# Kernel tuning notes

Measured on AMD Instinct MI355X. Metric: run time of the kernel, lower is better.

Reference implementation:

```python
import jax, jax.numpy as jnp
import numpy as np

N = 50000
E = 400000
D = 128            # embedding_dim
NUM_RBF = 20
CUT_OFF = 5.0
SILU_SCALE = 1.0 / 0.6


def scaled_silu(x):
    return jax.nn.silu(x) * SILU_SCALE


def cosine_cutoff(x):
    return 0.5 * (1.0 + jnp.cos(x * jnp.pi / CUT_OFF)) * (x < CUT_OFF).astype(x.dtype)


def setup_inputs() -> dict:
    key = jax.random.key(0)
    ks = jax.random.split(key, 10)
    vectorial_feat = jax.random.normal(ks[0], (N, D, 3), dtype=jnp.float32)
    scalar_feat = jax.random.normal(ks[1], (N, D), dtype=jnp.float32)
    node_pos = jax.random.uniform(ks[2], (N, 3), dtype=jnp.float32) * 10.0
    source = jax.random.randint(ks[3], (E,), 0, N)
    offset = jax.random.randint(ks[4], (E,), 1, N)  # avoid self-loops -> no zero distance
    target = (source + offset) % N
    edge_index = jnp.stack([source, target], axis=0).astype(jnp.int64)
    # scalar_feat_proj: Linear(D,D) -> ScaledSiLU -> Linear(D, 3D)
    W1 = jax.random.normal(ks[5], (D, D), dtype=jnp.float32) * (1.0 / np.sqrt(D))
    b1 = jnp.zeros((D,), dtype=jnp.float32)
    W2 = jax.random.normal(ks[6], (D, 3 * D), dtype=jnp.float32) * (1.0 / np.sqrt(D))
    b2 = jnp.zeros((3 * D,), dtype=jnp.float32)
    # rbf_proj: Linear(NUM_RBF, 3D)
    Wr = jax.random.normal(ks[7], (NUM_RBF, 3 * D), dtype=jnp.float32) * (1.0 / np.sqrt(NUM_RBF))
    br = jnp.zeros((3 * D,), dtype=jnp.float32)
    return {"vectorial_feat": vectorial_feat, "scalar_feat": scalar_feat,
            "node_pos": node_pos, "edge_index": edge_index,
            "W1": W1, "b1": b1, "W2": W2, "b2": b2, "Wr": Wr, "br": br}


def reference(vectorial_feat, scalar_feat, node_pos, edge_index, W1, b1, W2, b2, Wr, br):
    freqs = jnp.arange(1, NUM_RBF + 1, dtype=jnp.float32) * jnp.pi  # [NUM_RBF]
    source, target = edge_index[0], edge_index[1]

    # node-level scalar projection: [N, 3D]
    s = scaled_silu(scalar_feat @ W1 + b1) @ W2 + b2

    # per-edge geometry
    rel = node_pos[target] - node_pos[source]                 # [E, 3]
    dist = jnp.sqrt(jnp.sum(rel * rel, axis=-1))              # [E]
    dist_scaled = dist / CUT_OFF
    rbf = jnp.sin(freqs[None, :] * dist_scaled[:, None]) / dist[:, None]  # [E, NUM_RBF]

    filt = cosine_cutoff(rbf @ Wr + br)                       # [E, 3D]

    message = (s[source] * filt).reshape(E, D, 3)             # [E, D, 3]
    scalar_msg = message[..., 0]                              # [E, D]
    equiv_msg = message[..., 1]                               # [E, D]
    invar_msg = message[..., 2]                               # [E, D]

    scalar_message = jax.ops.segment_sum(scalar_msg, target, num_segments=N)  # [N, D]

    direction = rel / dist[:, None]                           # [E, 3]
    vec_msg = (invar_msg[:, :, None] * direction[:, None, :]
               + equiv_msg[:, :, None] * vectorial_feat[source])  # [E, D, 3]
    vectorial_message = jax.ops.segment_sum(vec_msg, target, num_segments=N)  # [N, D, 3]

    return vectorial_message, scalar_message
```

## Files before the change

### kernel.cpp

```cpp
#include <hip/hip_runtime.h>
#include <hip/hip_fp16.h>
#include <math.h>
#include <stddef.h>

#define D_DIM 128
#define NUM_RBF 20
typedef unsigned short ushort_t;
typedef unsigned int uint_t;
typedef _Float16 h2v __attribute__((ext_vector_type(2)));
typedef _Float16 half8_t __attribute__((ext_vector_type(8)));
typedef float float4_t __attribute__((ext_vector_type(4)));
constexpr float PI_F = 3.14159265358979323846f;
constexpr float CUT_OFF_F = 5.0f;
constexpr float SILU_SCALE_F = 1.0f / 0.6f;

__device__ __forceinline__ uint_t pack2h(float a, float b) {
  __half2 h2 = __floats2half2_rn(a, b);
  return *reinterpret_cast<uint_t*>(&h2);
}
__device__ __forceinline__ float h2f(ushort_t u) {
  __half h = __ushort_as_half(u);
  return __half2float(h);
}
__device__ __forceinline__ float h2f_lo(uint_t u) { return h2f((ushort_t)(u & 0xffffu)); }
__device__ __forceinline__ float h2f_hi(uint_t u) { return h2f((ushort_t)(u >> 16)); }
__device__ __forceinline__ h2v u2h2(uint_t u) {
  h2v r;
  __builtin_memcpy(&r, &u, 4);
  return r;
}

#if defined(__has_builtin)
#if __has_builtin(__builtin_amdgcn_fdot2)
#define HAVE_FDOT2 1
#endif
#endif

__device__ __forceinline__ float fdot2f(h2v a, h2v b, float c) {
#ifdef HAVE_FDOT2
  return __builtin_amdgcn_fdot2(a, b, c, false);
#else
  return c + (float)a.x * (float)b.x + (float)a.y * (float)b.y;
#endif
}

struct __align__(16) EdgeRec {
  uint_t rb[10];
  uint_t src;
  float dx, dy, dz;
  uint_t pad[2];
};

__device__ __forceinline__ void stage_wt(const float* __restrict__ W,
                                         _Float16* __restrict__ Wt, int t,
                                         int f4stride, int f4base) {
  const float4* Wv = reinterpret_cast<const float4*>(W);
#pragma unroll
  for (int i = 0; i < 8; ++i) {
    int pid = t + i * 256;
    int k = (pid >> 5) * 2;
    int nf = pid & 31;
    float4 a = Wv[(size_t)k * f4stride + f4base + nf];
    float4 b = Wv[(size_t)(k + 1) * f4stride + f4base + nf];
    const float av[4] = {a.x, a.y, a.z, a.w};
    const float bv[4] = {b.x, b.y, b.z, b.w};
    const int n0 = nf * 4;
#pragma unroll
    for (int j = 0; j < 4; ++j)
      *reinterpret_cast<uint_t*>(&Wt[(n0 + j) * 136 + k]) =
          pack2h(av[j], bv[j]);
  }
}

__global__ __launch_bounds__(256) void proj_kernel(
    const float* __restrict__ X, const float* __restrict__ W1,
    const float* __restrict__ b1, const float* __restrict__ W2,
    const float* __restrict__ b2, const float* __restrict__ vf,
    uint_t* __restrict__ merged, int* __restrict__ counts, int N) {
  __shared__ alignas(16) _Float16 smem[26112];
  _Float16* Xs = smem;
  _Float16* Wt = smem + 8704;

  const int t = threadIdx.x;
  const int w = t >> 6;
  const int l = t & 63;
  const int nb = blockIdx.x * 64;

  {
    int z = blockIdx.x * 256 + t;
    if (z < N) counts[z] = 0;
  }

  {
    const float4* Xv = reinterpret_cast<const float4*>(X);
#pragma unroll
    for (int i = 0; i < 8; ++i) {
      int g = t + i * 256;
      int row = g >> 5, k0 = (g & 31) * 4;
      int node = nb + row;
      float4 v = (node < N) ? Xv[(size_t)nb * 32 + g]
                            : make_float4(0.f, 0.f, 0.f, 0.f);
      uint_t* dst = reinterpret_cast<uint_t*>(&Xs[row * 136 + k0]);
      dst[0] = pack2h(v.x, v.y);
      dst[1] = pack2h(v.z, v.w);
    }
  }
  stage_wt(W1, Wt, t, 32, 0);
  __syncthreads();

  const int arow = w * 16 + (l & 15);
  const int koff = (l >> 4) * 8;
  const int bcol = l & 15;

  half8_t af[4];
#pragma unroll
  for (int s = 0; s < 4; ++s)
    af[s] = *reinterpret_cast<const half8_t*>(&Xs[arow * 136 + s * 32 + koff]);

  float4_t acc[8];
#pragma unroll
  for (int c = 0; c < 8; ++c) {
    float4_t a = {0.f, 0.f, 0.f, 0.f};
#pragma unroll
    for (int s = 0; s < 4; ++s) {
      half8_t bf = *reinterpret_cast<const half8_t*>(
          &Wt[(c * 16 + bcol) * 136 + s * 32 + koff]);
      a = __builtin_amdgcn_mfma_f32_16x16x32_f16(af[s], bf, a, 0, 0, 0);
    }
    acc[c] = a;
  }

  __syncthreads();

#pragma unroll
  for (int c = 0; c < 8; ++c) {
    const int col = c * 16 + bcol;
    const float bv = b1[col];
#pragma unroll
    for (int r = 0; r < 4; ++r) {
      const int row = w * 16 + (l >> 4) * 4 + r;
      float hv = acc[c][r] + bv;
      hv = hv * SILU_SCALE_F / (1.0f + expf(-hv));
      Xs[row * 136 + col] = (_Float16)hv;
    }
  }
  stage_wt(W2, Wt, t, 96, 0);
  __syncthreads();

  half8_t ha[4];
#pragma unroll
  for (int s = 0; s < 4; ++s)
    ha[s] = *reinterpret_cast<const half8_t*>(&Xs[arow * 136 + s * 32 + koff]);

  uint_t pk[3][8][2];
#pragma unroll
  for (int cn = 0; cn < 3; ++cn) {
    if (cn > 0) {
      __syncthreads();
      stage_wt(W2, Wt, t, 96, cn * 32);
      __syncthreads();
    }
#pragma unroll
    for (int c = 0; c < 8; ++c) {
      float4_t a = {0.f, 0.f, 0.f, 0.f};
#pragma unroll
      for (int s = 0; s < 4; ++s) {
        half8_t bf = *reinterpret_cast<const half8_t*>(
            &Wt[(c * 16 + bcol) * 136 + s * 32 + koff]);
        a = __builtin_amdgcn_mfma_f32_16x16x32_f16(ha[s], bf, a, 0, 0, 0);
      }
      const float bv = b2[cn * 128 + c * 16 + bcol];
      pk[cn][c][0] = pack2h(a[0] + bv, a[1] + bv);
      pk[cn][c][1] = pack2h(a[2] + bv, a[3] + bv);
    }
  }

  __syncthreads();
  ushort_t* sh = reinterpret_cast<ushort_t*>(smem);
  {
    const int rbase = w * 16 + (l >> 4) * 4;
#pragma unroll
    for (int cn = 0; cn < 3; ++cn)
#pragma unroll
      for (int c = 0; c < 8; ++c) {
        const int gcol = cn * 128 + c * 16 + bcol;
        sh[(rbase + 0) * 392 + gcol] = (ushort_t)(pk[cn][c][0] & 0xffffu);
        sh[(rbase + 1) * 392 + gcol] = (ushort_t)(pk[cn][c][0] >> 16);
        sh[(rbase + 2) * 392 + gcol] = (ushort_t)(pk[cn][c][1] & 0xffffu);
        sh[(rbase + 3) * 392 + gcol] = (ushort_t)(pk[cn][c][1] >> 16);
      }
  }
  __syncthreads();

#pragma unroll
  for (int k = 0; k < 8; ++k) {
    const int P = k * 256 + t;
    const int ln = P >> 5;
    const int cg = (P & 31) * 4;
    const int node = nb + ln;
    if (node < N) {
      const ushort_t* sp = &sh[ln * 392 + 3 * cg];
      uint2 sa = *reinterpret_cast<const uint2*>(sp);
      uint2 sb = *reinterpret_cast<const uint2*>(sp + 4);
      uint2 sc = *reinterpret_cast<const uint2*>(sp + 8);
      ushort_t s12[12];
      s12[0] = (ushort_t)(sa.x & 0xffffu);  s12[1] = (ushort_t)(sa.x >> 16);
      s12[2] = (ushort_t)(sa.y & 0xffffu);  s12[3] = (ushort_t)(sa.y >> 16);
      s12[4] = (ushort_t)(sb.x & 0xffffu);  s12[5] = (ushort_t)(sb.x >> 16);
      s12[6] = (ushort_t)(sb.y & 0xffffu);  s12[7] = (ushort_t)(sb.y >> 16);
      s12[8] = (ushort_t)(sc.x & 0xffffu);  s12[9] = (ushort_t)(sc.x >> 16);
      s12[10] = (ushort_t)(sc.y & 0xffffu); s12[11] = (ushort_t)(sc.y >> 16);

      const float4* vp =
          reinterpret_cast<const float4*>(vf + ((size_t)node * 128 + cg) * 3);
      float4 v0 = vp[0], v1 = vp[1], v2 = vp[2];
      float vv[12] = {v0.x, v0.y, v0.z, v0.w, v1.x, v1.y,
                      v1.z, v1.w, v2.x, v2.y, v2.z, v2.w};

      uint_t o[12];
#pragma unroll
      for (int j = 0; j < 4; ++j) {
        o[3 * j + 0] = (uint_t)s12[3 * j] | ((uint_t)s12[3 * j + 1] << 16);
        o[3 * j + 1] =
            (uint_t)s12[3 * j + 2] |
            ((uint_t)__half_as_ushort(__float2half_rn(vv[3 * j])) << 16);
        o[3 * j + 2] = pack2h(vv[3 * j + 1], vv[3 * j + 2]);
      }
      uint_t* mp = merged + ((size_t)node * 128 + cg) * 3;
      *reinterpret_cast<uint4*>(mp) = make_uint4(o[0], o[1], o[2], o[3]);
      *reinterpret_cast<uint4*>(mp + 4) = make_uint4(o[4], o[5], o[6], o[7]);
      *reinterpret_cast<uint4*>(mp + 8) = make_uint4(o[8], o[9], o[10], o[11]);
    }
  }
}

__global__ void hist_kernel(const int* __restrict__ tgt, int* __restrict__ counts,
                            int E) {
  int e = blockIdx.x * 256 + threadIdx.x;
  if (e < E) atomicAdd(&counts[tgt[e]], 1);
}

__global__ void chunk_sum_kernel(const int* __restrict__ counts,
                                 int* __restrict__ chunk_sums, int N) {
  __shared__ int red[256];
  int b = blockIdx.x, t = threadIdx.x;
  int base = b * 1024 + t * 4;
  int s = 0;
#pragma unroll
  for (int j = 0; j < 4; ++j) s += (base + j < N) ? counts[base + j] : 0;
  red[t] = s;
  __syncthreads();
  for (int off = 128; off > 0; off >>= 1) {
    if (t < off) red[t] += red[t + off];
    __syncthreads();
  }
  if (t == 0) chunk_sums[b] = red[0];
}

__global__ void scan_block_kernel(const int* __restrict__ counts,
                                  const int* __restrict__ chunk_sums,
                                  int* __restrict__ offsets,
                                  int* __restrict__ cursor, int N, int E) {
  __shared__ int part[256];
  __shared__ int chunk_base_sh;
  int b = blockIdx.x, t = threadIdx.x;
  if (t < 64) {
    int v = (t < b) ? chunk_sums[t] : 0;
#pragma unroll
    for (int off = 32; off > 0; off >>= 1) v += __shfl_down(v, off);
    if (t == 0) chunk_base_sh = v;
  }
  int base = b * 1024 + t * 4;
  int v[4];
#pragma unroll
  for (int j = 0; j < 4; ++j) v[j] = (base + j < N) ? counts[base + j] : 0;
  int local = v[0] + v[1] + v[2] + v[3];
  part[t] = local;
  __syncthreads();
  for (int off = 1; off < 256; off <<= 1) {
    int x = 0;
    if (t >= off) x = part[t - off];
    __syncthreads();
    if (t >= off) part[t] += x;
    __syncthreads();
  }
  int run = chunk_base_sh + (part[t] - local);
#pragma unroll
  for (int j = 0; j < 4; ++j) {
    if (base + j < N) {
      offsets[base + j] = run;
      cursor[base + j] = run;
      run += v[j];
    }
  }
  if (b == 0 && t == 0) offsets[N] = E;
}

__global__ void edge_geom_kernel(const float* __restrict__ pos,
                                 const int* __restrict__ src,
                                 const int* __restrict__ tgt,
                                 int* __restrict__ cursor,
                                 EdgeRec* __restrict__ recs, int E) {
  int e = blockIdx.x * 256 + threadIdx.x;
  if (e >= E) return;
  const int sn = src[e];
  const int tn = tgt[e];
  const float rx = pos[tn * 3 + 0] - pos[sn * 3 + 0];
  const float ry = pos[tn * 3 + 1] - pos[sn * 3 + 1];
  const float rz = pos[tn * 3 + 2] - pos[sn * 3 + 2];
  const float dist = sqrtf(rx * rx + ry * ry + rz * rz);
  const float inv = 1.0f / dist;

  const float ang = dist * (PI_F / CUT_OFF_F);
  float s1, c1;
  sincosf(ang, &s1, &c1);
  float sk = s1, ck = c1;
  float rb[NUM_RBF];
  rb[0] = s1 * inv;
#pragma unroll
  for (int r = 1; r < NUM_RBF; ++r) {
    float sn2 = sk * c1 + ck * s1;
    ck = ck * c1 - sk * s1;
    sk = sn2;
    rb[r] = sk * inv;
  }

  const int p = atomicAdd(&cursor[tn], 1);
  uint_t us[10];
#pragma unroll
  for (int q = 0; q < 10; ++q) us[q] = pack2h(rb[2 * q], rb[2 * q + 1]);
  uint_t* o = reinterpret_cast<uint_t*>(&recs[p]);
  *reinterpret_cast<uint4*>(o) = make_uint4(us[0], us[1], us[2], us[3]);
  *reinterpret_cast<uint4*>(o + 4) = make_uint4(us[4], us[5], us[6], us[7]);
  *reinterpret_cast<uint4*>(o + 8) =
      make_uint4(us[8], us[9], (uint_t)sn, __float_as_uint(rx * inv));
  *reinterpret_cast<uint4*>(o + 12) =
      make_uint4(__float_as_uint(ry * inv), __float_as_uint(rz * inv), 0u, 0u);
}

#define NODES_PER_BLOCK 8

__device__ __forceinline__ float cutoff_f(float x) {
#if defined(__has_builtin)
#if __has_builtin(__builtin_amdgcn_cosf)
  float c = __builtin_amdgcn_cosf(x * 0.1f);
#else
  float c = __cosf(x * (PI_F / CUT_OFF_F));
#endif
#else
  float c = __cosf(x * (PI_F / CUT_OFF_F));
#endif
  return (x < CUT_OFF_F) ? 0.5f + 0.5f * c : 0.f;
}

__device__ __forceinline__ void edge_body(const EdgeRec& e, uint_t su0,
                                          uint_t su1, uint_t su2,
                                          const h2v* wr0h, const h2v* wr1h,
                                          const h2v* wr2h, float br0, float br1,
                                          float br2, float& accs, float& av0,
                                          float& av1, float& av2) {
  float f0 = br0, f1 = br1, f2 = br2;
#pragma unroll
  for (int q = 0; q < 10; ++q) {
    h2v r = u2h2(e.rb[q]);
    f0 = fdot2f(r, wr0h[q], f0);
    f1 = fdot2f(r, wr1h[q], f1);
    f2 = fdot2f(r, wr2h[q], f2);
  }
  f0 = cutoff_f(f0);
  f1 = cutoff_f(f1);
  f2 = cutoff_f(f2);
  const float m0 = h2f_lo(su0) * f0;
  const float m1 = h2f_hi(su0) * f1;
  const float m2 = h2f_lo(su1) * f2;
  accs += m0;
  av0 += m2 * e.dx + m1 * h2f_hi(su1);
  av1 += m2 * e.dy + m1 * h2f_lo(su2);
  av2 += m2 * e.dz + m1 * h2f_hi(su2);
}

__global__ __launch_bounds__(128) void node_kernel(
    const uint_t* __restrict__ merged, const EdgeRec* __restrict__ recs,
    const int* __restrict__ offsets, const float* __restrict__ Wr,
    const float* __restrict__ br, float* __restrict__ out, int N) {
  const int d = threadIdx.x;
  const int d3 = 3 * d;

  h2v wr0h[10], wr1h[10], wr2h[10];
#pragma unroll
  for (int q = 0; q < 10; ++q) {
    h2v w;
    w.x = (_Float16)Wr[(2 * q) * 384 + d3 + 0];
    w.y = (_Float16)Wr[(2 * q + 1) * 384 + d3 + 0];
    wr0h[q] = w;
    w.x = (_Float16)Wr[(2 * q) * 384 + d3 + 1];
    w.y = (_Float16)Wr[(2 * q + 1) * 384 + d3 + 1];
    wr1h[q] = w;
    w.x = (_Float16)Wr[(2 * q) * 384 + d3 + 2];
    w.y = (_Float16)Wr[(2 * q + 1) * 384 + d3 + 2];
    wr2h[q] = w;
  }
  const float br0 = br[d3 + 0];
  const float br1 = br[d3 + 1];
  const float br2 = br[d3 + 2];

  for (int nn = 0; nn < NODES_PER_BLOCK; ++nn) {
    const int n = blockIdx.x * NODES_PER_BLOCK + nn;
    if (n >= N) break;

    const int start = offsets[n];
    const int end = offsets[n + 1];

    float accs = 0.f, av0 = 0.f, av1 = 0.f, av2 = 0.f;

    int i = start;
    for (; i + 4 <= end; i += 4) {
      const int i0 = __builtin_amdgcn_readfirstlane(i);
      const EdgeRec& eA = recs[i0];
      const EdgeRec& eB = recs[i0 + 1];
      const EdgeRec& eC = recs[i0 + 2];
      const EdgeRec& eD = recs[i0 + 3];
      const uint_t* mpA = merged + (size_t)eA.src * 384 + d3;
      const uint_t* mpB = merged + (size_t)eB.src * 384 + d3;
      const uint_t* mpC = merged + (size_t)eC.src * 384 + d3;
      const uint_t* mpD = merged + (size_t)eD.src * 384 + d3;
      const uint_t suA0 = mpA[0], suA1 = mpA[1], suA2 = mpA[2];
      const uint_t suB0 = mpB[0], suB1 = mpB[1], suB2 = mpB[2];
      const uint_t suC0 = mpC[0], suC1 = mpC[1], suC2 = mpC[2];
      const uint_t suD0 = mpD[0], suD1 = mpD[1], suD2 = mpD[2];

      edge_body(eA, suA0, suA1, suA2, wr0h, wr1h, wr2h, br0, br1, br2, accs,
                av0, av1, av2);
      edge_body(eB, suB0, suB1, suB2, wr0h, wr1h, wr2h, br0, br1, br2, accs,
                av0, av1, av2);
      edge_body(eC, suC0, suC1, suC2, wr0h, wr1h, wr2h, br0, br1, br2, accs,
                av0, av1, av2);
      edge_body(eD, suD0, suD1, suD2, wr0h, wr1h, wr2h, br0, br1, br2, accs,
                av0, av1, av2);
    }
    for (; i < end; ++i) {
      const int i0 = __builtin_amdgcn_readfirstlane(i);
      const EdgeRec& eA = recs[i0];
      const uint_t* mpA = merged + (size_t)eA.src * 384 + d3;
      const uint_t suA0 = mpA[0], suA1 = mpA[1], suA2 = mpA[2];
      edge_body(eA, suA0, suA1, suA2, wr0h, wr1h, wr2h, br0, br1, br2, accs,
                av0, av1, av2);
    }

    out[(size_t)n * 384 + d3 + 0] = av0;
    out[(size_t)n * 384 + d3 + 1] = av1;
    out[(size_t)n * 384 + d3 + 2] = av2;
    out[(size_t)N * 384 + (size_t)n * 128 + d] = accs;
  }
}

extern "C" void kernel_launch(void* const* d_in, const int* in_sizes, int n_in,
                              void* d_out, int out_size, void* d_ws,
                              size_t ws_size, hipStream_t stream) {
  const float* vf  = (const float*)d_in[0];
  const float* X   = (const float*)d_in[1];
  const float* pos = (const float*)d_in[2];
  const int* ei    = (const int*)d_in[3];
  const float* W1  = (const float*)d_in[4];
  const float* b1  = (const float*)d_in[5];
  const float* W2  = (const float*)d_in[6];
  const float* b2  = (const float*)d_in[7];
  const float* Wr  = (const float*)d_in[8];
  const float* br  = (const float*)d_in[9];

  const int N = in_sizes[1] / D_DIM;
  const int E = in_sizes[3] / 2;
  const int* srcI = ei;
  const int* tgtI = ei + E;
  float* out = (float*)d_out;

  char* w = (char*)d_ws;
  EdgeRec* recs  = (EdgeRec*)w; w += (size_t)E * sizeof(EdgeRec);
  uint_t* merged = (uint_t*)w;  w += (size_t)N * 128 * 3 * sizeof(uint_t);
  int* counts    = (int*)w;     w += (size_t)N * sizeof(int);
  int* offsets   = (int*)w;     w += (size_t)(N + 1) * sizeof(int);
  int* cursor    = (int*)w;     w += (size_t)N * sizeof(int);
  int* chunks    = (int*)w;     w += 64 * sizeof(int);

  const int nch = (N + 1023) / 1024;

  proj_kernel<<<(N + 63) / 64, 256, 0, stream>>>(X, W1, b1, W2, b2, vf, merged,
                                                 counts, N);
  hist_kernel<<<(E + 255) / 256, 256, 0, stream>>>(tgtI, counts, E);
  chunk_sum_kernel<<<nch, 256, 0, stream>>>(counts, chunks, N);
  scan_block_kernel<<<nch, 256, 0, stream>>>(counts, chunks, offsets, cursor,
                                             N, E);
  edge_geom_kernel<<<(E + 255) / 256, 256, 0, stream>>>(pos, srcI, tgtI, cursor,
                                                        recs, E);
  node_kernel<<<(N + NODES_PER_BLOCK - 1) / NODES_PER_BLOCK, 128, 0, stream>>>(
      merged, recs, offsets, Wr, br, out, N);
}
```

Before: 274.3 us.

## Fuse histogram, scan and edge geometry into one cooperative kernel

Replaces four separate kernel launches (histogram, chunk sum, block scan, edge geometry) with a single cooperative kernel of 512 blocks that uses grid-wide syncs between phases and grid-stride loops. The aim is to cut launch overhead and inter-kernel gaps on the CSR-building path. In exchange, work per phase is spread over fewer blocks, and the grid syncs add their own cost.

```diff
diff --git a/kernel.cpp b/kernel.cpp
--- a/kernel.cpp
+++ b/kernel.cpp
@@ -1,7 +1,10 @@
 #include <hip/hip_runtime.h>
+#include <hip/hip_cooperative_groups.h>
 #include <hip/hip_fp16.h>
 #include <math.h>
 #include <stddef.h>
+
+namespace cg = cooperative_groups;
 
 #define D_DIM 128
 #define NUM_RBF 20
@@ -196,10 +199,10 @@
   for (int k = 0; k < 8; ++k) {
     const int P = k * 256 + t;
     const int ln = P >> 5;
-    const int cg = (P & 31) * 4;
+    const int cg2 = (P & 31) * 4;
     const int node = nb + ln;
     if (node < N) {
-      const ushort_t* sp = &sh[ln * 392 + 3 * cg];
+      const ushort_t* sp = &sh[ln * 392 + 3 * cg2];
       uint2 sa = *reinterpret_cast<const uint2*>(sp);
       uint2 sb = *reinterpret_cast<const uint2*>(sp + 4);
       uint2 sc = *reinterpret_cast<const uint2*>(sp + 8);
@@ -212,7 +215,7 @@
       s12[10] = (ushort_t)(sc.y & 0xffffu); s12[11] = (ushort_t)(sc.y >> 16);
 
       const float4* vp =
-          reinterpret_cast<const float4*>(vf + ((size_t)node * 128 + cg) * 3);
+          reinterpret_cast<const float4*>(vf + ((size_t)node * 128 + cg2) * 3);
       float4 v0 = vp[0], v1 = vp[1], v2 = vp[2];
       float vv[12] = {v0.x, v0.y, v0.z, v0.w, v1.x, v1.y,
                       v1.z, v1.w, v2.x, v2.y, v2.z, v2.w};
@@ -226,7 +229,7 @@
             ((uint_t)__half_as_ushort(__float2half_rn(vv[3 * j])) << 16);
         o[3 * j + 2] = pack2h(vv[3 * j + 1], vv[3 * j + 2]);
       }
-      uint_t* mp = merged + ((size_t)node * 128 + cg) * 3;
+      uint_t* mp = merged + ((size_t)node * 128 + cg2) * 3;
       *reinterpret_cast<uint4*>(mp) = make_uint4(o[0], o[1], o[2], o[3]);
       *reinterpret_cast<uint4*>(mp + 4) = make_uint4(o[4], o[5], o[6], o[7]);
       *reinterpret_cast<uint4*>(mp + 8) = make_uint4(o[8], o[9], o[10], o[11]);
@@ -234,108 +237,112 @@
   }
 }
 
-__global__ void hist_kernel(const int* __restrict__ tgt, int* __restrict__ counts,
-                            int E) {
-  int e = blockIdx.x * 256 + threadIdx.x;
-  if (e < E) atomicAdd(&counts[tgt[e]], 1);
-}
-
-__global__ void chunk_sum_kernel(const int* __restrict__ counts,
-                                 int* __restrict__ chunk_sums, int N) {
+__global__ __launch_bounds__(256) void csr_geom_kernel(
+    const float* __restrict__ pos, const int* __restrict__ src,
+    const int* __restrict__ tgt, int* __restrict__ counts,
+    int* __restrict__ chunk_sums, int* __restrict__ offsets,
+    int* __restrict__ cursor, EdgeRec* __restrict__ recs, int N, int E,
+    int nch) {
+  cg::grid_group grid = cg::this_grid();
   __shared__ int red[256];
-  int b = blockIdx.x, t = threadIdx.x;
-  int base = b * 1024 + t * 4;
-  int s = 0;
-#pragma unroll
-  for (int j = 0; j < 4; ++j) s += (base + j < N) ? counts[base + j] : 0;
-  red[t] = s;
-  __syncthreads();
-  for (int off = 128; off > 0; off >>= 1) {
-    if (t < off) red[t] += red[t + off];
-    __syncthreads();
-  }
-  if (t == 0) chunk_sums[b] = red[0];
-}
-
-__global__ void scan_block_kernel(const int* __restrict__ counts,
-                                  const int* __restrict__ chunk_sums,
-                                  int* __restrict__ offsets,
-                                  int* __restrict__ cursor, int N, int E) {
   __shared__ int part[256];
   __shared__ int chunk_base_sh;
-  int b = blockIdx.x, t = threadIdx.x;
-  if (t < 64) {
-    int v = (t < b) ? chunk_sums[t] : 0;
-#pragma unroll
-    for (int off = 32; off > 0; off >>= 1) v += __shfl_down(v, off);
-    if (t == 0) chunk_base_sh = v;
-  }
-  int base = b * 1024 + t * 4;
-  int v[4];
-#pragma unroll
-  for (int j = 0; j < 4; ++j) v[j] = (base + j < N) ? counts[base + j] : 0;
-  int local = v[0] + v[1] + v[2] + v[3];
-  part[t] = local;
-  __syncthreads();
-  for (int off = 1; off < 256; off <<= 1) {
-    int x = 0;
-    if (t >= off) x = part[t - off];
+
+  const int t = threadIdx.x;
+  const int nblk = gridDim.x;
+  const int gstride = nblk * 256;
+
+  for (int e = blockIdx.x * 256 + t; e < E; e += gstride)
+    atomicAdd(&counts[tgt[e]], 1);
+  grid.sync();
+
+  for (int c = blockIdx.x; c < nch; c += nblk) {
+    int base = c * 1024 + t * 4;
+    int s = 0;
+#pragma unroll
+    for (int j = 0; j < 4; ++j) s += (base + j < N) ? counts[base + j] : 0;
+    red[t] = s;
     __syncthreads();
-    if (t >= off) part[t] += x;
+    for (int off = 128; off > 0; off >>= 1) {
+      if (t < off) red[t] += red[t + off];
+      __syncthreads();
+    }
+    if (t == 0) chunk_sums[c] = red[0];
     __syncthreads();
   }
-  int run = chunk_base_sh + (part[t] - local);
-#pragma unroll
-  for (int j = 0; j < 4; ++j) {
-    if (base + j < N) {
-      offsets[base + j] = run;
-      cursor[base + j] = run;
-      run += v[j];
-    }
-  }
-  if (b == 0 && t == 0) offsets[N] = E;
-}
-
-__global__ void edge_geom_kernel(const float* __restrict__ pos,
-                                 const int* __restrict__ src,
-                                 const int* __restrict__ tgt,
-                                 int* __restrict__ cursor,
-                                 EdgeRec* __restrict__ recs, int E) {
-  int e = blockIdx.x * 256 + threadIdx.x;
-  if (e >= E) return;
-  const int sn = src[e];
-  const int tn = tgt[e];
-  const float rx = pos[tn * 3 + 0] - pos[sn * 3 + 0];
-  const float ry = pos[tn * 3 + 1] - pos[sn * 3 + 1];
-  const float rz = pos[tn * 3 + 2] - pos[sn * 3 + 2];
-  const float dist = sqrtf(rx * rx + ry * ry + rz * rz);
-  const float inv = 1.0f / dist;
-
-  const float ang = dist * (PI_F / CUT_OFF_F);
-  float s1, c1;
-  sincosf(ang, &s1, &c1);
-  float sk = s1, ck = c1;
-  float rb[NUM_RBF];
-  rb[0] = s1 * inv;
-#pragma unroll
-  for (int r = 1; r < NUM_RBF; ++r) {
-    float sn2 = sk * c1 + ck * s1;
-    ck = ck * c1 - sk * s1;
-    sk = sn2;
-    rb[r] = sk * inv;
-  }
-
-  const int p = atomicAdd(&cursor[tn], 1);
-  uint_t us[10];
-#pragma unroll
-  for (int q = 0; q < 10; ++q) us[q] = pack2h(rb[2 * q], rb[2 * q + 1]);
-  uint_t* o = reinterpret_cast<uint_t*>(&recs[p]);
-  *reinterpret_cast<uint4*>(o) = make_uint4(us[0], us[1], us[2], us[3]);
-  *reinterpret_cast<uint4*>(o + 4) = make_uint4(us[4], us[5], us[6], us[7]);
-  *reinterpret_cast<uint4*>(o + 8) =
-      make_uint4(us[8], us[9], (uint_t)sn, __float_as_uint(rx * inv));
-  *reinterpret_cast<uint4*>(o + 12) =
-      make_uint4(__float_as_uint(ry * inv), __float_as_uint(rz * inv), 0u, 0u);
+  grid.sync();
+
+  for (int c = blockIdx.x; c < nch; c += nblk) {
+    if (t < 64) {
+      int v = (t < c) ? chunk_sums[t] : 0;
+#pragma unroll
+      for (int off = 32; off > 0; off >>= 1) v += __shfl_down(v, off);
+      if (t == 0) chunk_base_sh = v;
+    }
+    int base = c * 1024 + t * 4;
+    int v[4];
+#pragma unroll
+    for (int j = 0; j < 4; ++j) v[j] = (base + j < N) ? counts[base + j] : 0;
+    int local = v[0] + v[1] + v[2] + v[3];
+    part[t] = local;
+    __syncthreads();
+    for (int off = 1; off < 256; off <<= 1) {
+      int x = 0;
+      if (t >= off) x = part[t - off];
+      __syncthreads();
+      if (t >= off) part[t] += x;
+      __syncthreads();
+    }
+    int run = chunk_base_sh + (part[t] - local);
+#pragma unroll
+    for (int j = 0; j < 4; ++j) {
+      if (base + j < N) {
+        offsets[base + j] = run;
+        cursor[base + j] = run;
+        run += v[j];
+      }
+    }
+    __syncthreads();
+  }
+  if (blockIdx.x == 0 && t == 0) offsets[N] = E;
+  grid.sync();
+
+  for (int e = blockIdx.x * 256 + t; e < E; e += gstride) {
+    const int sn = src[e];
+    const int tn = tgt[e];
+    const float rx = pos[tn * 3 + 0] - pos[sn * 3 + 0];
+    const float ry = pos[tn * 3 + 1] - pos[sn * 3 + 1];
+    const float rz = pos[tn * 3 + 2] - pos[sn * 3 + 2];
+    const float dist = sqrtf(rx * rx + ry * ry + rz * rz);
+    const float inv = 1.0f / dist;
+
+    const float ang = dist * (PI_F / CUT_OFF_F);
+    float s1, c1;
+    sincosf(ang, &s1, &c1);
+    float sk = s1, ck = c1;
+    float rb[NUM_RBF];
+    rb[0] = s1 * inv;
+#pragma unroll
+    for (int r = 1; r < NUM_RBF; ++r) {
+      float sn2 = sk * c1 + ck * s1;
+      ck = ck * c1 - sk * s1;
+      sk = sn2;
+      rb[r] = sk * inv;
+    }
+
+    const int p = atomicAdd(&cursor[tn], 1);
+    uint_t us[10];
+#pragma unroll
+    for (int q = 0; q < 10; ++q) us[q] = pack2h(rb[2 * q], rb[2 * q + 1]);
+    uint_t* o = reinterpret_cast<uint_t*>(&recs[p]);
+    *reinterpret_cast<uint4*>(o) = make_uint4(us[0], us[1], us[2], us[3]);
+    *reinterpret_cast<uint4*>(o + 4) = make_uint4(us[4], us[5], us[6], us[7]);
+    *reinterpret_cast<uint4*>(o + 8) =
+        make_uint4(us[8], us[9], (uint_t)sn, __float_as_uint(rx * inv));
+    *reinterpret_cast<uint4*>(o + 12) =
+        make_uint4(__float_as_uint(ry * inv), __float_as_uint(rz * inv), 0u,
+                   0u);
+  }
 }
 
 #define NODES_PER_BLOCK 8
@@ -482,16 +489,29 @@
   int* cursor    = (int*)w;     w += (size_t)N * sizeof(int);
   int* chunks    = (int*)w;     w += 64 * sizeof(int);
 
-  const int nch = (N + 1023) / 1024;
+  int Nv = N, Ev = E;
+  int nch = (N + 1023) / 1024;
 
   proj_kernel<<<(N + 63) / 64, 256, 0, stream>>>(X, W1, b1, W2, b2, vf, merged,
                                                  counts, N);
-  hist_kernel<<<(E + 255) / 256, 256, 0, stream>>>(tgtI, counts, E);
-  chunk_sum_kernel<<<nch, 256, 0, stream>>>(counts, chunks, N);
-  scan_block_kernel<<<nch, 256, 0, stream>>>(counts, chunks, offsets, cursor,
-                                             N, E);
-  edge_geom_kernel<<<(E + 255) / 256, 256, 0, stream>>>(pos, srcI, tgtI, cursor,
-                                                        recs, E);
+
+  {
+    const float* pos_a = pos;
+    const int* src_a = srcI;
+    const int* tgt_a = tgtI;
+    int* counts_a = counts;
+    int* chunks_a = chunks;
+    int* offsets_a = offsets;
+    int* cursor_a = cursor;
+    EdgeRec* recs_a = recs;
+    void* args[] = {(void*)&pos_a,    (void*)&src_a,    (void*)&tgt_a,
+                    (void*)&counts_a, (void*)&chunks_a, (void*)&offsets_a,
+                    (void*)&cursor_a, (void*)&recs_a,   (void*)&Nv,
+                    (void*)&Ev,       (void*)&nch};
+    hipLaunchCooperativeKernel((void*)csr_geom_kernel, dim3(512), dim3(256),
+                               args, 0, stream);
+  }
+
   node_kernel<<<(N + NODES_PER_BLOCK - 1) / NODES_PER_BLOCK, 128, 0, stream>>>(
       merged, recs, offsets, Wr, br, out, N);
 }
```

After: 435.0 us. +58.6%, slower.
